# Kernel tuning notes

Hardware: AMD Instinct MI355X
Metric: run time of the kernel (lower is better)

The kernel has to match this reference:

```python
import jax, jax.numpy as jnp
import numpy as np

H = 2048          # hidden_size
F = 1408          # moe_intermediate_size
E = 64            # n_routed_experts
TOP_K = 6         # num_experts_per_tok
CAP = 512         # per-expert capacity (mean load ~192; overflow prob ~0)
SCALE = 1.0       # routed_scaling_factor
F_SH = 2 * F      # shared-expert intermediate (n_shared_experts=2)
B, S = 1, 2048


def setup_inputs() -> dict:
    key = jax.random.key(0)
    ks = jax.random.split(key, 8)
    s = 0.02
    return {
        "hidden_states": jax.random.normal(ks[0], (B, S, H), jnp.float32),
        "gate_w":  jax.random.normal(ks[1], (E, H), jnp.float32) * s,
        "w_gate":  jax.random.normal(ks[2], (E, H, F), jnp.float32) * s,
        "w_up":    jax.random.normal(ks[3], (E, H, F), jnp.float32) * s,
        "w_down":  jax.random.normal(ks[4], (E, F, H), jnp.float32) * s,
        "sh_gate": jax.random.normal(ks[5], (F_SH, H), jnp.float32) * s,
        "sh_up":   jax.random.normal(ks[6], (F_SH, H), jnp.float32) * s,
        "sh_down": jax.random.normal(ks[7], (H, F_SH), jnp.float32) * s,
    }


def reference(hidden_states, gate_w, w_gate, w_up, w_down, sh_gate, sh_up, sh_down):
    b, s, _ = hidden_states.shape
    x = hidden_states.reshape(-1, H)                       # [T, H]
    T = x.shape[0]

    # ---- gate: fp32 logits -> softmax -> top-k, scaled ----
    logits = x.astype(jnp.float32) @ gate_w.astype(jnp.float32).T   # [T, E]
    scores = jax.nn.softmax(logits, axis=-1)
    topk_w, topk_idx = jax.lax.top_k(scores, TOP_K)        # [T, K] (order irrelevant: summed)
    topk_w = topk_w * SCALE

    # ---- dispatch: sort expanded tokens by expert, scatter into [E, CAP, H] ----
    eid = topk_idx.reshape(-1)                             # [T*K]
    x_exp = jnp.repeat(x, TOP_K, axis=0)                   # [T*K, H] (token t repeated K times)
    order = jnp.argsort(eid)                               # stable sort by expert id
    eid_s = eid[order]
    counts = jnp.bincount(eid, length=E)
    starts = jnp.cumsum(counts) - counts                   # exclusive prefix sums
    pos = jnp.arange(T * TOP_K) - starts[eid_s]            # slot within expert
    valid = pos < CAP
    pos_c = jnp.where(valid, pos, CAP)                     # overflow -> scratch slot CAP
    buf = jnp.zeros((E, CAP + 1, H), x.dtype).at[eid_s, pos_c].set(x_exp[order])

    # ---- grouped expert SwiGLU MLP (grouped GEMM as batched einsum) ----
    g = jax.nn.silu(jnp.einsum('ech,ehf->ecf', buf, w_gate))
    u = jnp.einsum('ech,ehf->ecf', buf, w_up)
    d = jnp.einsum('ecf,efh->ech', g * u, w_down)          # [E, CAP+1, H]

    # ---- combine: gather, unsort, weighted sum over top-k ----
    out_s = jnp.where(valid[:, None], d[eid_s, pos_c], 0.0)
    out_exp = jnp.zeros_like(out_s).at[order].set(out_s)   # reverse_shuffle
    y = jnp.einsum('tkh,tk->th', out_exp.reshape(T, TOP_K, H), topk_w)
    y = y.astype(x.dtype).reshape(b, s, H)

    # ---- shared experts residual (dense SwiGLU MLP on identity) ----
    gs = jax.nn.silu(hidden_states @ sh_gate.T)
    us = hidden_states @ sh_up.T
    y = y + (gs * us) @ sh_down.T
    return y
```

## Files before the change

kernel.cpp:

```cpp
#include <hip/hip_runtime.h>
#include <hip/hip_bf16.h>

#define H 2048
#define FDIM 1408
#define NE 64
#define CAP 512
#define NTOK 2048
#define FSH 2816

typedef float  f32x4  __attribute__((ext_vector_type(4)));
typedef short  s16x8  __attribute__((ext_vector_type(8)));
typedef unsigned short u16;
typedef u16    u16x4v __attribute__((ext_vector_type(4)));

__device__ __forceinline__ u16 f2bf(float f) {
    union { float f; unsigned u; } v; v.f = f;
    unsigned u = v.u;
    u += 0x7fffu + ((u >> 16) & 1u);
    return (u16)(u >> 16);
}
__device__ __forceinline__ float bf2f(u16 b) {
    union { unsigned u; float f; } v; v.u = ((unsigned)b) << 16;
    return v.f;
}
__device__ __forceinline__ int swze(int row) {
    return (((row & 7) ^ ((row >> 3) & 7)) << 3);
}
__device__ __forceinline__ void wr4(u16* dst, float a, float b, float c, float d) {
    u16x4v v; v[0] = f2bf(a); v[1] = f2bf(b); v[2] = f2bf(c); v[3] = f2bf(d);
    *(u16x4v*)dst = v;
}

__global__ __launch_bounds__(256) void xcvt(const float* __restrict__ x, u16* __restrict__ xb) {
    int i = blockIdx.x * 256 + threadIdx.x;
    const float4 a = ((const float4*)x)[2 * i];
    const float4 b = ((const float4*)x)[2 * i + 1];
    u16 v[8] = { f2bf(a.x), f2bf(a.y), f2bf(a.z), f2bf(a.w),
                 f2bf(b.x), f2bf(b.y), f2bf(b.z), f2bf(b.w) };
    *(s16x8*)(xb + (size_t)i * 8) = *(s16x8*)v;
}

__global__ void init_cnt(int* __restrict__ c) { c[threadIdx.x] = 0; }

__global__ __launch_bounds__(64) void gate_topk(
    const float* __restrict__ xg, const float* __restrict__ gw,
    int* __restrict__ cnt, int* __restrict__ tok_of,
    int* __restrict__ slot_enc, float* __restrict__ tw)
{
    const int t = blockIdx.x;
    const int lane = threadIdx.x;
    __shared__ float4 xs[512];
    const float4* xr = (const float4*)(xg + (size_t)t * H);
    #pragma unroll
    for (int i = 0; i < 8; ++i) xs[i * 64 + lane] = xr[i * 64 + lane];
    __syncthreads();

    const float4* gr = (const float4*)(gw + (size_t)lane * H);
    float acc = 0.f;
    #pragma unroll 4
    for (int i = 0; i < 512; ++i) {
        float4 a = xs[i], b = gr[i];
        acc += a.x * b.x + a.y * b.y + a.z * b.z + a.w * b.w;
    }
    float m = acc;
    #pragma unroll
    for (int off = 32; off; off >>= 1) m = fmaxf(m, __shfl_xor(m, off));
    float p = __expf(acc - m);
    float s = p;
    #pragma unroll
    for (int off = 32; off; off >>= 1) s += __shfl_xor(s, off);
    p = p / s;

    float myw = 0.f; int mye = 0;
    float v = p;
    for (int k = 0; k < 6; ++k) {
        float bv = v; int bi = lane;
        #pragma unroll
        for (int off = 32; off; off >>= 1) {
            float ov = __shfl_xor(bv, off);
            int   oi = __shfl_xor(bi, off);
            if (ov > bv || (ov == bv && oi < bi)) { bv = ov; bi = oi; }
        }
        if (lane == k)  { myw = bv; mye = bi; }
        if (lane == bi) v = -1.f;
    }
    if (lane < 6) {
        int slot = atomicAdd(&cnt[mye], 1);
        int enc = -1;
        if (slot < CAP) { tok_of[mye * CAP + slot] = t; enc = mye * CAP + slot; }
        slot_enc[t * 6 + lane] = enc;
        tw[t * 6 + lane] = myw;
    }
}

template<bool ROUTED>
__global__ __launch_bounds__(256) void dual_gemm(
    const u16* __restrict__ xbf, const int* __restrict__ tok_of,
    const int* __restrict__ cnt_arr, const float* __restrict__ wg,
    const float* __restrict__ wu, u16* __restrict__ act, int Fd)
{
    __shared__ u16 As[256 * 64];
    __shared__ u16 Bgs[32 * 64];
    __shared__ u16 Bus[32 * 64];

    const int e = blockIdx.z;
    int cnt;
    if constexpr (ROUTED) { cnt = cnt_arr[e]; cnt = cnt < CAP ? cnt : CAP; }
    else cnt = NTOK;
    const int m0 = blockIdx.y * 256;
    if (m0 >= cnt) return;
    const int f0 = blockIdx.x * 32;

    const float* wg_e = wg;
    const float* wu_e = wu;
    u16* act_e = act;
    const int* tok = nullptr;
    if constexpr (ROUTED) {
        wg_e += (size_t)e * H * Fd;
        wu_e += (size_t)e * H * Fd;
        act_e += (size_t)e * CAP * Fd;
        tok = tok_of + e * CAP;
    }

    const int tid = threadIdx.x;
    const int lane = tid & 63;
    const int wv = tid >> 6;

    const int ac = tid & 7;
    const u16* arow[8];
    int arl[8];
    #pragma unroll
    for (int it = 0; it < 8; ++it) {
        int row = it * 32 + (tid >> 3);
        arl[it] = row;
        int srow = m0 + row;
        int tkn;
        if constexpr (ROUTED) tkn = (srow < cnt) ? tok[srow] : 0;
        else tkn = srow;
        arow[it] = xbf + (size_t)tkn * H;
    }
    const int bb = tid & 127;
    const int bn4 = bb & 7;
    const int bkb = bb >> 3;
    const float* bsrcR = ((tid < 128) ? wg_e : wu_e) + (size_t)f0 + bn4 * 4 + (size_t)bkb * 4 * Fd;
    const int dr = bb >> 2;
    const int dc = (bb & 3) * 4;
    const float* bsrcD = ((tid < 128) ? wg_e : wu_e) + (size_t)(f0 + dr) * H + dc * 4;

    f32x4 accg[4][2], accu[4][2];
    const f32x4 zero4 = {0.f, 0.f, 0.f, 0.f};
    #pragma unroll
    for (int i = 0; i < 4; ++i)
        #pragma unroll
        for (int j = 0; j < 2; ++j) { accg[i][j] = zero4; accu[i][j] = zero4; }

    s16x8 aR[8];
    float4 bR[4];

    #pragma unroll
    for (int it = 0; it < 8; ++it) aR[it] = *(const s16x8*)(arow[it] + ac * 8);
    if constexpr (ROUTED) {
        #pragma unroll
        for (int r = 0; r < 4; ++r) bR[r] = *(const float4*)(bsrcR + (size_t)r * Fd);
    } else {
        #pragma unroll
        for (int q = 0; q < 4; ++q) bR[q] = *(const float4*)(bsrcD + q * 4);
    }

    for (int kt = 0; kt < H / 64; ++kt) {
        #pragma unroll
        for (int it = 0; it < 8; ++it)
            *(s16x8*)&As[arl[it] * 64 + ((ac * 8) ^ swze(arl[it]))] = aR[it];
        u16* Bdst = (tid < 128) ? Bgs : Bus;
        if constexpr (ROUTED) {
            #pragma unroll
            for (int j = 0; j < 4; ++j) {
                int rr = bn4 * 4 + j;
                wr4(&Bdst[rr * 64 + ((bkb * 4) ^ swze(rr))], bR[0][j], bR[1][j], bR[2][j], bR[3][j]);
            }
        } else {
            #pragma unroll
            for (int q = 0; q < 4; ++q)
                wr4(&Bdst[dr * 64 + (((dc + q) * 4) ^ swze(dr))], bR[q].x, bR[q].y, bR[q].z, bR[q].w);
        }
        __syncthreads();

        if (kt + 1 < H / 64) {
            const int ko = (kt + 1) * 64;
            #pragma unroll
            for (int it = 0; it < 8; ++it) aR[it] = *(const s16x8*)(arow[it] + ko + ac * 8);
            if constexpr (ROUTED) {
                #pragma unroll
                for (int r = 0; r < 4; ++r) bR[r] = *(const float4*)(bsrcR + (size_t)(ko + r) * Fd);
            } else {
                #pragma unroll
                for (int q = 0; q < 4; ++q) bR[q] = *(const float4*)(bsrcD + ko + q * 4);
            }
        }

        __builtin_amdgcn_s_setprio(1);
        #pragma unroll
        for (int kk = 0; kk < 2; ++kk) {
            int ko = kk * 32 + (lane >> 4) * 8;
            s16x8 a[4], bg[2], bu[2];
            #pragma unroll
            for (int mi = 0; mi < 4; ++mi) {
                int r = wv * 64 + mi * 16 + (lane & 15);
                a[mi] = *(const s16x8*)&As[r * 64 + (ko ^ swze(r))];
            }
            #pragma unroll
            for (int ni = 0; ni < 2; ++ni) {
                int r = ni * 16 + (lane & 15);
                bg[ni] = *(const s16x8*)&Bgs[r * 64 + (ko ^ swze(r))];
                bu[ni] = *(const s16x8*)&Bus[r * 64 + (ko ^ swze(r))];
            }
            #pragma unroll
            for (int mi = 0; mi < 4; ++mi)
                #pragma unroll
                for (int ni = 0; ni < 2; ++ni) {
                    accg[mi][ni] = __builtin_amdgcn_mfma_f32_16x16x32_bf16(a[mi], bg[ni], accg[mi][ni], 0, 0, 0);
                    accu[mi][ni] = __builtin_amdgcn_mfma_f32_16x16x32_bf16(a[mi], bu[ni], accu[mi][ni], 0, 0, 0);
                }
        }
        __builtin_amdgcn_s_setprio(0);
        __syncthreads();
    }

    #pragma unroll
    for (int mi = 0; mi < 4; ++mi)
        #pragma unroll
        for (int ni = 0; ni < 2; ++ni)
            #pragma unroll
            for (int r = 0; r < 4; ++r) {
                int srow = m0 + wv * 64 + mi * 16 + (lane >> 4) * 4 + r;
                if (srow < cnt) {
                    int fc = f0 + ni * 16 + (lane & 15);
                    float g = accg[mi][ni][r], u = accu[mi][ni][r];
                    float aa = (g / (1.f + __expf(-g))) * u;
                    int fs = (fc & ~63) | ((fc & 63) ^ swze(srow));
                    act_e[(size_t)srow * Fd + fs] = f2bf(aa);
                }
            }
}

template<bool ROUTED>
__global__ __launch_bounds__(256) void down_gemm(
    const u16* __restrict__ actA, const float* __restrict__ wdn,
    void* __restrict__ outp, const int* __restrict__ cnt_arr, int Kd)
{
    __shared__ u16 As[256 * 64];
    __shared__ u16 Bs[64 * 64];

    const int e = blockIdx.z;
    int cnt;
    if constexpr (ROUTED) { cnt = cnt_arr[e]; cnt = cnt < CAP ? cnt : CAP; }
    else cnt = NTOK;
    const int m0 = blockIdx.y * 256;
    if (m0 >= cnt) return;
    const int n0 = blockIdx.x * 64;

    const u16* A_e = actA;
    const float* B_e = wdn;
    if constexpr (ROUTED) {
        A_e += (size_t)e * CAP * Kd;
        B_e += (size_t)e * Kd * H;
    }

    const int tid = threadIdx.x, lane = tid & 63, wv = tid >> 6;
    const int NT = Kd / 64;

    const int ac = tid & 7;
    int arl[8];
    const u16* arow[8];
    #pragma unroll
    for (int it = 0; it < 8; ++it) {
        int row = it * 32 + (tid >> 3);
        arl[it] = row;
        arow[it] = A_e + (size_t)(m0 + row) * Kd;
    }
    const int bn4 = tid & 15;
    const int bkb = tid >> 4;
    const float* bsrcR = B_e + (size_t)n0 + bn4 * 4 + (size_t)bkb * 4 * H;
    const int dr = tid >> 2;
    const int dc = (tid & 3) * 4;
    const float* bsrcD = B_e + (size_t)(n0 + dr) * FSH + dc * 4;

    f32x4 acc[4][4];
    const f32x4 zero4 = {0.f, 0.f, 0.f, 0.f};
    #pragma unroll
    for (int i = 0; i < 4; ++i)
        #pragma unroll
        for (int j = 0; j < 4; ++j) acc[i][j] = zero4;

    s16x8 aR[8];
    float4 bR[4];

    #pragma unroll
    for (int it = 0; it < 8; ++it) aR[it] = *(const s16x8*)(arow[it] + ac * 8);
    if constexpr (ROUTED) {
        #pragma unroll
        for (int r = 0; r < 4; ++r) bR[r] = *(const float4*)(bsrcR + (size_t)r * H);
    } else {
        #pragma unroll
        for (int q = 0; q < 4; ++q) bR[q] = *(const float4*)(bsrcD + q * 4);
    }

    for (int kt = 0; kt < NT; ++kt) {
        #pragma unroll
        for (int it = 0; it < 8; ++it)
            *(s16x8*)&As[arl[it] * 64 + (ac * 8)] = aR[it];
        if constexpr (ROUTED) {
            #pragma unroll
            for (int j = 0; j < 4; ++j) {
                int rr = bn4 * 4 + j;
                wr4(&Bs[rr * 64 + ((bkb * 4) ^ swze(rr))], bR[0][j], bR[1][j], bR[2][j], bR[3][j]);
            }
        } else {
            #pragma unroll
            for (int q = 0; q < 4; ++q)
                wr4(&Bs[dr * 64 + (((dc + q) * 4) ^ swze(dr))], bR[q].x, bR[q].y, bR[q].z, bR[q].w);
        }
        __syncthreads();

        if (kt + 1 < NT) {
            const int ko = (kt + 1) * 64;
            #pragma unroll
            for (int it = 0; it < 8; ++it) aR[it] = *(const s16x8*)(arow[it] + ko + ac * 8);
            if constexpr (ROUTED) {
                #pragma unroll
                for (int r = 0; r < 4; ++r) bR[r] = *(const float4*)(bsrcR + (size_t)(ko + r) * H);
            } else {
                #pragma unroll
                for (int q = 0; q < 4; ++q) bR[q] = *(const float4*)(bsrcD + ko + q * 4);
            }
        }

        __builtin_amdgcn_s_setprio(1);
        #pragma unroll
        for (int kk = 0; kk < 2; ++kk) {
            int ko = kk * 32 + (lane >> 4) * 8;
            s16x8 a[4], b[4];
            #pragma unroll
            for (int mi = 0; mi < 4; ++mi) {
                int r = wv * 64 + mi * 16 + (lane & 15);
                a[mi] = *(const s16x8*)&As[r * 64 + (ko ^ swze(r))];
            }
            #pragma unroll
            for (int ni = 0; ni < 4; ++ni) {
                int r = ni * 16 + (lane & 15);
                b[ni] = *(const s16x8*)&Bs[r * 64 + (ko ^ swze(r))];
            }
            #pragma unroll
            for (int mi = 0; mi < 4; ++mi)
                #pragma unroll
                for (int ni = 0; ni < 4; ++ni)
                    acc[mi][ni] = __builtin_amdgcn_mfma_f32_16x16x32_bf16(a[mi], b[ni], acc[mi][ni], 0, 0, 0);
        }
        __builtin_amdgcn_s_setprio(0);
        __syncthreads();
    }

    #pragma unroll
    for (int mi = 0; mi < 4; ++mi)
        #pragma unroll
        for (int ni = 0; ni < 4; ++ni)
            #pragma unroll
            for (int r = 0; r < 4; ++r) {
                int srow = m0 + wv * 64 + mi * 16 + (lane >> 4) * 4 + r;
                if (srow < cnt) {
                    int col = n0 + ni * 16 + (lane & 15);
                    float vv = acc[mi][ni][r];
                    if constexpr (ROUTED)
                        ((u16*)outp)[(size_t)e * CAP * H + (size_t)srow * H + col] = f2bf(vv);
                    else
                        ((float*)outp)[(size_t)srow * H + col] = vv;
                }
            }
}

__global__ __launch_bounds__(256) void combine(
    float* __restrict__ y, const u16* __restrict__ d,
    const int* __restrict__ slot_enc, const float* __restrict__ tw)
{
    const int t = blockIdx.x, tid = threadIdx.x;
    int enc[6]; float w[6];
    #pragma unroll
    for (int k = 0; k < 6; ++k) {
        enc[k] = slot_enc[t * 6 + k];
        w[k] = tw[t * 6 + k];
    }
    float4* yrow = (float4*)(y + (size_t)t * H);
    #pragma unroll
    for (int it = 0; it < 2; ++it) {
        int h4 = it * 256 + tid;
        float4 acc = yrow[h4];
        #pragma unroll
        for (int k = 0; k < 6; ++k) {
            if (enc[k] >= 0) {
                ushort4 dv = ((const ushort4*)(d + (size_t)enc[k] * H))[h4];
                acc.x += w[k] * bf2f(dv.x);
                acc.y += w[k] * bf2f(dv.y);
                acc.z += w[k] * bf2f(dv.z);
                acc.w += w[k] * bf2f(dv.w);
            }
        }
        yrow[h4] = acc;
    }
}

extern "C" void kernel_launch(void* const* d_in, const int* in_sizes, int n_in,
                              void* d_out, int out_size, void* d_ws, size_t ws_size,
                              hipStream_t stream) {
    const float* x       = (const float*)d_in[0];
    const float* gw      = (const float*)d_in[1];
    const float* w_gate  = (const float*)d_in[2];
    const float* w_up    = (const float*)d_in[3];
    const float* w_down  = (const float*)d_in[4];
    const float* sh_gate = (const float*)d_in[5];
    const float* sh_up   = (const float*)d_in[6];
    const float* sh_down = (const float*)d_in[7];
    float* y = (float*)d_out;

    char* wsb = (char*)d_ws;
    int*   cnt      = (int*)(wsb + 0);
    int*   tok_of   = (int*)(wsb + 512);
    int*   slot_enc = (int*)(wsb + 512 + 131072);
    float* tw       = (float*)(wsb + 512 + 131072 + 49152);
    u16*   act      = (u16*)(wsb + 230144);
    u16*   actsh    = (u16*)(wsb + 230144 + 92274688);
    u16*   dbuf     = (u16*)(wsb + 230144 + 92274688 + 11534336);
    u16*   xbf      = dbuf;

    init_cnt<<<1, 64, 0, stream>>>(cnt);
    xcvt<<<NTOK * H / 8 / 256, 256, 0, stream>>>(x, xbf);
    gate_topk<<<NTOK, 64, 0, stream>>>(x, gw, cnt, tok_of, slot_enc, tw);
    dual_gemm<true><<<dim3(FDIM / 32, 2, NE), 256, 0, stream>>>(
        xbf, tok_of, cnt, w_gate, w_up, act, FDIM);
    dual_gemm<false><<<dim3(FSH / 32, NTOK / 256, 1), 256, 0, stream>>>(
        xbf, nullptr, nullptr, sh_gate, sh_up, actsh, FSH);
    down_gemm<true><<<dim3(H / 64, 2, NE), 256, 0, stream>>>(
        act, w_down, (void*)dbuf, cnt, FDIM);
    down_gemm<false><<<dim3(H / 64, NTOK / 256, 1), 256, 0, stream>>>(
        actsh, sh_down, (void*)y, nullptr, FSH);
    combine<<<NTOK, 256, 0, stream>>>(y, dbuf, slot_enc, tw);
}
```

Before: 937.0 us.

## Double-buffer LDS tiles with k-major layout and two-deep register prefetch in GEMMs

Both the dual (gate/up) and down GEMM kernels now keep two LDS buffers. The loop stores the next tile while computing the current one and loads tile kt+2 into registers, which removes one barrier per k-step. The LDS layout moves from row-major with an XOR swizzle to a k8-major [k8][row][8] layout with XOR on the B rows. Each thread now loads one full A row, which drops the swizzled activation output, and the shared-expert grids are transposed so M blocks vary fastest for weight reuse. The cost is doubled LDS use, which may reduce occupancy despite the launch_bounds hint of 2 blocks, plus a custom barrier that waits only on lgkmcnt.

New measurement: 1.107 ms. 1.18x slower.

```diff
diff --git a/kernel.cpp b/kernel.cpp
--- a/kernel.cpp
+++ b/kernel.cpp
@@ -23,13 +23,9 @@
     union { unsigned u; float f; } v; v.u = ((unsigned)b) << 16;
     return v.f;
 }
-__device__ __forceinline__ int swze(int row) {
-    return (((row & 7) ^ ((row >> 3) & 7)) << 3);
-}
-__device__ __forceinline__ void wr4(u16* dst, float a, float b, float c, float d) {
-    u16x4v v; v[0] = f2bf(a); v[1] = f2bf(b); v[2] = f2bf(c); v[3] = f2bf(d);
-    *(u16x4v*)dst = v;
-}
+
+#define BAR() do { asm volatile("s_waitcnt lgkmcnt(0)" ::: "memory"); \
+                   __builtin_amdgcn_s_barrier(); } while (0)
 
 __global__ __launch_bounds__(256) void xcvt(const float* __restrict__ x, u16* __restrict__ xb) {
     int i = blockIdx.x * 256 + threadIdx.x;
@@ -94,59 +90,62 @@
 }
 
 template<bool ROUTED>
-__global__ __launch_bounds__(256) void dual_gemm(
+__global__ __launch_bounds__(256, 2) void dual_gemm(
     const u16* __restrict__ xbf, const int* __restrict__ tok_of,
     const int* __restrict__ cnt_arr, const float* __restrict__ wg,
     const float* __restrict__ wu, u16* __restrict__ act, int Fd)
 {
-    __shared__ u16 As[256 * 64];
-    __shared__ u16 Bgs[32 * 64];
-    __shared__ u16 Bus[32 * 64];
-
-    const int e = blockIdx.z;
-    int cnt;
-    if constexpr (ROUTED) { cnt = cnt_arr[e]; cnt = cnt < CAP ? cnt : CAP; }
-    else cnt = NTOK;
-    const int m0 = blockIdx.y * 256;
-    if (m0 >= cnt) return;
-    const int f0 = blockIdx.x * 32;
+    __shared__ u16 As[2][8][256][8];
+    __shared__ u16 Bs[2][2][8][32][8];
+
+    int e = 0, cnt, m0, f0;
+    if constexpr (ROUTED) {
+        e = blockIdx.z;
+        cnt = cnt_arr[e]; cnt = cnt < CAP ? cnt : CAP;
+        f0 = blockIdx.x * 32; m0 = blockIdx.y * 256;
+        if (m0 >= cnt) return;
+    } else {
+        cnt = NTOK;
+        m0 = blockIdx.x * 256; f0 = blockIdx.y * 32;
+    }
 
     const float* wg_e = wg;
     const float* wu_e = wu;
     u16* act_e = act;
-    const int* tok = nullptr;
     if constexpr (ROUTED) {
         wg_e += (size_t)e * H * Fd;
         wu_e += (size_t)e * H * Fd;
         act_e += (size_t)e * CAP * Fd;
-        tok = tok_of + e * CAP;
     }
 
     const int tid = threadIdx.x;
     const int lane = tid & 63;
     const int wv = tid >> 6;
 
-    const int ac = tid & 7;
-    const u16* arow[8];
-    int arl[8];
-    #pragma unroll
-    for (int it = 0; it < 8; ++it) {
-        int row = it * 32 + (tid >> 3);
-        arl[it] = row;
-        int srow = m0 + row;
-        int tkn;
-        if constexpr (ROUTED) tkn = (srow < cnt) ? tok[srow] : 0;
-        else tkn = srow;
-        arow[it] = xbf + (size_t)tkn * H;
-    }
+    const u16* aptr;
+    {
+        int srow = m0 + tid;
+        if constexpr (ROUTED) {
+            const int* tok = tok_of + e * CAP;
+            aptr = xbf + (size_t)tok[srow < cnt ? srow : 0] * H;
+        } else {
+            aptr = xbf + (size_t)srow * H;
+        }
+    }
+    const int mat = tid >> 7;
     const int bb = tid & 127;
-    const int bn4 = bb & 7;
-    const int bkb = bb >> 3;
-    const float* bsrcR = ((tid < 128) ? wg_e : wu_e) + (size_t)f0 + bn4 * 4 + (size_t)bkb * 4 * Fd;
-    const int dr = bb >> 2;
-    const int dc = (bb & 3) * 4;
-    const float* bsrcD = ((tid < 128) ? wg_e : wu_e) + (size_t)(f0 + dr) * H + dc * 4;
-
+    const float* bsrc;
+    int n4 = 0, kq = 0, br = 0, bc = 0;
+    if constexpr (ROUTED) {
+        n4 = bb & 7; kq = bb >> 3;
+        bsrc = (mat ? wu_e : wg_e) + (size_t)(kq * 4) * Fd + f0 + n4 * 4;
+    } else {
+        br = bb >> 2; bc = bb & 3;
+        bsrc = (mat ? wu_e : wg_e) + (size_t)(f0 + br) * H + bc * 16;
+    }
+
+    s16x8 aR[8];
+    f32x4 bR[4];
     f32x4 accg[4][2], accu[4][2];
     const f32x4 zero4 = {0.f, 0.f, 0.f, 0.f};
     #pragma unroll
@@ -154,65 +153,62 @@
         #pragma unroll
         for (int j = 0; j < 2; ++j) { accg[i][j] = zero4; accu[i][j] = zero4; }
 
-    s16x8 aR[8];
-    float4 bR[4];
-
-    #pragma unroll
-    for (int it = 0; it < 8; ++it) aR[it] = *(const s16x8*)(arow[it] + ac * 8);
-    if constexpr (ROUTED) {
-        #pragma unroll
-        for (int r = 0; r < 4; ++r) bR[r] = *(const float4*)(bsrcR + (size_t)r * Fd);
-    } else {
-        #pragma unroll
-        for (int q = 0; q < 4; ++q) bR[q] = *(const float4*)(bsrcD + q * 4);
-    }
-
+    auto LOAD = [&](int kt) {
+        #pragma unroll
+        for (int q = 0; q < 8; ++q) aR[q] = *(const s16x8*)(aptr + kt * 64 + q * 8);
+        if constexpr (ROUTED) {
+            #pragma unroll
+            for (int j = 0; j < 4; ++j)
+                bR[j] = *(const f32x4*)(bsrc + ((size_t)kt * 64 + j) * Fd);
+        } else {
+            #pragma unroll
+            for (int q = 0; q < 4; ++q)
+                bR[q] = *(const f32x4*)(bsrc + kt * 64 + q * 4);
+        }
+    };
+    auto STORE = [&](int b) {
+        #pragma unroll
+        for (int q = 0; q < 8; ++q) *(s16x8*)&As[b][q][tid][0] = aR[q];
+        if constexpr (ROUTED) {
+            const int k8 = kq >> 1, ko = (kq & 1) * 4;
+            #pragma unroll
+            for (int c = 0; c < 4; ++c) {
+                u16x4v v; v[0] = f2bf(bR[0][c]); v[1] = f2bf(bR[1][c]);
+                          v[2] = f2bf(bR[2][c]); v[3] = f2bf(bR[3][c]);
+                *(u16x4v*)&Bs[b][mat][k8][(n4 * 4 + c) ^ k8][ko] = v;
+            }
+        } else {
+            #pragma unroll
+            for (int h = 0; h < 2; ++h) {
+                const int k8 = bc * 2 + h;
+                u16 v[8];
+                f32x4 x0 = bR[h * 2], x1 = bR[h * 2 + 1];
+                v[0]=f2bf(x0[0]); v[1]=f2bf(x0[1]); v[2]=f2bf(x0[2]); v[3]=f2bf(x0[3]);
+                v[4]=f2bf(x1[0]); v[5]=f2bf(x1[1]); v[6]=f2bf(x1[2]); v[7]=f2bf(x1[3]);
+                *(s16x8*)&Bs[b][mat][k8][br ^ k8][0] = *(s16x8*)v;
+            }
+        }
+    };
+
+    LOAD(0); STORE(0); LOAD(1);
+    BAR();
     for (int kt = 0; kt < H / 64; ++kt) {
-        #pragma unroll
-        for (int it = 0; it < 8; ++it)
-            *(s16x8*)&As[arl[it] * 64 + ((ac * 8) ^ swze(arl[it]))] = aR[it];
-        u16* Bdst = (tid < 128) ? Bgs : Bus;
-        if constexpr (ROUTED) {
-            #pragma unroll
-            for (int j = 0; j < 4; ++j) {
-                int rr = bn4 * 4 + j;
-                wr4(&Bdst[rr * 64 + ((bkb * 4) ^ swze(rr))], bR[0][j], bR[1][j], bR[2][j], bR[3][j]);
-            }
-        } else {
-            #pragma unroll
-            for (int q = 0; q < 4; ++q)
-                wr4(&Bdst[dr * 64 + (((dc + q) * 4) ^ swze(dr))], bR[q].x, bR[q].y, bR[q].z, bR[q].w);
-        }
-        __syncthreads();
-
-        if (kt + 1 < H / 64) {
-            const int ko = (kt + 1) * 64;
-            #pragma unroll
-            for (int it = 0; it < 8; ++it) aR[it] = *(const s16x8*)(arow[it] + ko + ac * 8);
-            if constexpr (ROUTED) {
-                #pragma unroll
-                for (int r = 0; r < 4; ++r) bR[r] = *(const float4*)(bsrcR + (size_t)(ko + r) * Fd);
-            } else {
-                #pragma unroll
-                for (int q = 0; q < 4; ++q) bR[q] = *(const float4*)(bsrcD + ko + q * 4);
-            }
-        }
-
+        const int b = kt & 1;
+        if (kt + 1 < H / 64) STORE(b ^ 1);
+        if (kt + 2 < H / 64) LOAD(kt + 2);
         __builtin_amdgcn_s_setprio(1);
         #pragma unroll
         for (int kk = 0; kk < 2; ++kk) {
-            int ko = kk * 32 + (lane >> 4) * 8;
+            const int k8 = kk * 4 + (lane >> 4);
             s16x8 a[4], bg[2], bu[2];
             #pragma unroll
-            for (int mi = 0; mi < 4; ++mi) {
-                int r = wv * 64 + mi * 16 + (lane & 15);
-                a[mi] = *(const s16x8*)&As[r * 64 + (ko ^ swze(r))];
-            }
+            for (int mi = 0; mi < 4; ++mi)
+                a[mi] = *(const s16x8*)&As[b][k8][wv * 64 + mi * 16 + (lane & 15)][0];
             #pragma unroll
             for (int ni = 0; ni < 2; ++ni) {
-                int r = ni * 16 + (lane & 15);
-                bg[ni] = *(const s16x8*)&Bgs[r * 64 + (ko ^ swze(r))];
-                bu[ni] = *(const s16x8*)&Bus[r * 64 + (ko ^ swze(r))];
+                const int np = (ni * 16 + (lane & 15)) ^ k8;
+                bg[ni] = *(const s16x8*)&Bs[b][0][k8][np][0];
+                bu[ni] = *(const s16x8*)&Bs[b][1][k8][np][0];
             }
             #pragma unroll
             for (int mi = 0; mi < 4; ++mi)
@@ -223,7 +219,7 @@
                 }
         }
         __builtin_amdgcn_s_setprio(0);
-        __syncthreads();
+        BAR();
     }
 
     #pragma unroll
@@ -237,27 +233,29 @@
                     int fc = f0 + ni * 16 + (lane & 15);
                     float g = accg[mi][ni][r], u = accu[mi][ni][r];
                     float aa = (g / (1.f + __expf(-g))) * u;
-                    int fs = (fc & ~63) | ((fc & 63) ^ swze(srow));
-                    act_e[(size_t)srow * Fd + fs] = f2bf(aa);
+                    act_e[(size_t)srow * Fd + fc] = f2bf(aa);
                 }
             }
 }
 
 template<bool ROUTED>
-__global__ __launch_bounds__(256) void down_gemm(
+__global__ __launch_bounds__(256, 2) void down_gemm(
     const u16* __restrict__ actA, const float* __restrict__ wdn,
     void* __restrict__ outp, const int* __restrict__ cnt_arr, int Kd)
 {
-    __shared__ u16 As[256 * 64];
-    __shared__ u16 Bs[64 * 64];
-
-    const int e = blockIdx.z;
-    int cnt;
-    if constexpr (ROUTED) { cnt = cnt_arr[e]; cnt = cnt < CAP ? cnt : CAP; }
-    else cnt = NTOK;
-    const int m0 = blockIdx.y * 256;
-    if (m0 >= cnt) return;
-    const int n0 = blockIdx.x * 64;
+    __shared__ u16 As[2][8][256][8];
+    __shared__ u16 Bs[2][8][64][8];
+
+    int e = 0, cnt, m0, n0;
+    if constexpr (ROUTED) {
+        e = blockIdx.z;
+        cnt = cnt_arr[e]; cnt = cnt < CAP ? cnt : CAP;
+        n0 = blockIdx.x * 64; m0 = blockIdx.y * 256;
+        if (m0 >= cnt) return;
+    } else {
+        cnt = NTOK;
+        m0 = blockIdx.x * 256; n0 = blockIdx.y * 64;
+    }
 
     const u16* A_e = actA;
     const float* B_e = wdn;
@@ -265,26 +263,27 @@
         A_e += (size_t)e * CAP * Kd;
         B_e += (size_t)e * Kd * H;
     }
-
+    const int NT = Kd / 64;
     const int tid = threadIdx.x, lane = tid & 63, wv = tid >> 6;
-    const int NT = Kd / 64;
-
-    const int ac = tid & 7;
-    int arl[8];
-    const u16* arow[8];
-    #pragma unroll
-    for (int it = 0; it < 8; ++it) {
-        int row = it * 32 + (tid >> 3);
-        arl[it] = row;
-        arow[it] = A_e + (size_t)(m0 + row) * Kd;
-    }
-    const int bn4 = tid & 15;
-    const int bkb = tid >> 4;
-    const float* bsrcR = B_e + (size_t)n0 + bn4 * 4 + (size_t)bkb * 4 * H;
-    const int dr = tid >> 2;
-    const int dc = (tid & 3) * 4;
-    const float* bsrcD = B_e + (size_t)(n0 + dr) * FSH + dc * 4;
-
+
+    const u16* aptr;
+    {
+        int row = m0 + tid;
+        if constexpr (ROUTED) aptr = A_e + (size_t)(row < cnt ? row : m0) * Kd;
+        else aptr = A_e + (size_t)row * Kd;
+    }
+    const float* bsrc;
+    int n4 = 0, kq = 0, br = 0, bc = 0;
+    if constexpr (ROUTED) {
+        n4 = tid & 15; kq = tid >> 4;
+        bsrc = B_e + (size_t)(kq * 4) * H + n0 + n4 * 4;
+    } else {
+        br = tid >> 2; bc = tid & 3;
+        bsrc = B_e + (size_t)(n0 + br) * FSH + bc * 16;
+    }
+
+    s16x8 aR[8];
+    f32x4 bR[4];
     f32x4 acc[4][4];
     const f32x4 zero4 = {0.f, 0.f, 0.f, 0.f};
     #pragma unroll
@@ -292,72 +291,68 @@
         #pragma unroll
         for (int j = 0; j < 4; ++j) acc[i][j] = zero4;
 
-    s16x8 aR[8];
-    float4 bR[4];
-
-    #pragma unroll
-    for (int it = 0; it < 8; ++it) aR[it] = *(const s16x8*)(arow[it] + ac * 8);
-    if constexpr (ROUTED) {
-        #pragma unroll
-        for (int r = 0; r < 4; ++r) bR[r] = *(const float4*)(bsrcR + (size_t)r * H);
-    } else {
-        #pragma unroll
-        for (int q = 0; q < 4; ++q) bR[q] = *(const float4*)(bsrcD + q * 4);
-    }
-
+    auto LOAD = [&](int kt) {
+        #pragma unroll
+        for (int q = 0; q < 8; ++q) aR[q] = *(const s16x8*)(aptr + kt * 64 + q * 8);
+        if constexpr (ROUTED) {
+            #pragma unroll
+            for (int j = 0; j < 4; ++j)
+                bR[j] = *(const f32x4*)(bsrc + ((size_t)kt * 64 + j) * H);
+        } else {
+            #pragma unroll
+            for (int q = 0; q < 4; ++q)
+                bR[q] = *(const f32x4*)(bsrc + kt * 64 + q * 4);
+        }
+    };
+    auto STORE = [&](int b) {
+        #pragma unroll
+        for (int q = 0; q < 8; ++q) *(s16x8*)&As[b][q][tid][0] = aR[q];
+        if constexpr (ROUTED) {
+            const int k8 = kq >> 1, ko = (kq & 1) * 4;
+            #pragma unroll
+            for (int c = 0; c < 4; ++c) {
+                u16x4v v; v[0] = f2bf(bR[0][c]); v[1] = f2bf(bR[1][c]);
+                          v[2] = f2bf(bR[2][c]); v[3] = f2bf(bR[3][c]);
+                *(u16x4v*)&Bs[b][k8][(n4 * 4 + c) ^ k8][ko] = v;
+            }
+        } else {
+            #pragma unroll
+            for (int h = 0; h < 2; ++h) {
+                const int k8 = bc * 2 + h;
+                u16 v[8];
+                f32x4 x0 = bR[h * 2], x1 = bR[h * 2 + 1];
+                v[0]=f2bf(x0[0]); v[1]=f2bf(x0[1]); v[2]=f2bf(x0[2]); v[3]=f2bf(x0[3]);
+                v[4]=f2bf(x1[0]); v[5]=f2bf(x1[1]); v[6]=f2bf(x1[2]); v[7]=f2bf(x1[3]);
+                *(s16x8*)&Bs[b][k8][br ^ k8][0] = *(s16x8*)v;
+            }
+        }
+    };
+
+    LOAD(0); STORE(0); LOAD(1);
+    BAR();
     for (int kt = 0; kt < NT; ++kt) {
-        #pragma unroll
-        for (int it = 0; it < 8; ++it)
-            *(s16x8*)&As[arl[it] * 64 + (ac * 8)] = aR[it];
-        if constexpr (ROUTED) {
-            #pragma unroll
-            for (int j = 0; j < 4; ++j) {
-                int rr = bn4 * 4 + j;
-                wr4(&Bs[rr * 64 + ((bkb * 4) ^ swze(rr))], bR[0][j], bR[1][j], bR[2][j], bR[3][j]);
-            }
-        } else {
-            #pragma unroll
-            for (int q = 0; q < 4; ++q)
-                wr4(&Bs[dr * 64 + (((dc + q) * 4) ^ swze(dr))], bR[q].x, bR[q].y, bR[q].z, bR[q].w);
-        }
-        __syncthreads();
-
-        if (kt + 1 < NT) {
-            const int ko = (kt + 1) * 64;
-            #pragma unroll
-            for (int it = 0; it < 8; ++it) aR[it] = *(const s16x8*)(arow[it] + ko + ac * 8);
-            if constexpr (ROUTED) {
-                #pragma unroll
-                for (int r = 0; r < 4; ++r) bR[r] = *(const float4*)(bsrcR + (size_t)(ko + r) * H);
-            } else {
-                #pragma unroll
-                for (int q = 0; q < 4; ++q) bR[q] = *(const float4*)(bsrcD + ko + q * 4);
-            }
-        }
-
+        const int b = kt & 1;
+        if (kt + 1 < NT) STORE(b ^ 1);
+        if (kt + 2 < NT) LOAD(kt + 2);
         __builtin_amdgcn_s_setprio(1);
         #pragma unroll
         for (int kk = 0; kk < 2; ++kk) {
-            int ko = kk * 32 + (lane >> 4) * 8;
-            s16x8 a[4], b[4];
-            #pragma unroll
-            for (int mi = 0; mi < 4; ++mi) {
-                int r = wv * 64 + mi * 16 + (lane & 15);
-                a[mi] = *(const s16x8*)&As[r * 64 + (ko ^ swze(r))];
-            }
-            #pragma unroll
-            for (int ni = 0; ni < 4; ++ni) {
-                int r = ni * 16 + (lane & 15);
-                b[ni] = *(const s16x8*)&Bs[r * 64 + (ko ^ swze(r))];
-            }
+            const int k8 = kk * 4 + (lane >> 4);
+            s16x8 a[4], bf[4];
+            #pragma unroll
+            for (int mi = 0; mi < 4; ++mi)
+                a[mi] = *(const s16x8*)&As[b][k8][wv * 64 + mi * 16 + (lane & 15)][0];
+            #pragma unroll
+            for (int ni = 0; ni < 4; ++ni)
+                bf[ni] = *(const s16x8*)&Bs[b][k8][(ni * 16 + (lane & 15)) ^ k8][0];
             #pragma unroll
             for (int mi = 0; mi < 4; ++mi)
                 #pragma unroll
                 for (int ni = 0; ni < 4; ++ni)
-                    acc[mi][ni] = __builtin_amdgcn_mfma_f32_16x16x32_bf16(a[mi], b[ni], acc[mi][ni], 0, 0, 0);
+                    acc[mi][ni] = __builtin_amdgcn_mfma_f32_16x16x32_bf16(a[mi], bf[ni], acc[mi][ni], 0, 0, 0);
         }
         __builtin_amdgcn_s_setprio(0);
-        __syncthreads();
+        BAR();
     }
 
     #pragma unroll
@@ -436,11 +431,11 @@
     gate_topk<<<NTOK, 64, 0, stream>>>(x, gw, cnt, tok_of, slot_enc, tw);
     dual_gemm<true><<<dim3(FDIM / 32, 2, NE), 256, 0, stream>>>(
         xbf, tok_of, cnt, w_gate, w_up, act, FDIM);
-    dual_gemm<false><<<dim3(FSH / 32, NTOK / 256, 1), 256, 0, stream>>>(
+    dual_gemm<false><<<dim3(NTOK / 256, FSH / 32, 1), 256, 0, stream>>>(
         xbf, nullptr, nullptr, sh_gate, sh_up, actsh, FSH);
     down_gemm<true><<<dim3(H / 64, 2, NE), 256, 0, stream>>>(
         act, w_down, (void*)dbuf, cnt, FDIM);
-    down_gemm<false><<<dim3(H / 64, NTOK / 256, 1), 256, 0, stream>>>(
+    down_gemm<false><<<dim3(NTOK / 256, H / 64, 1), 256, 0, stream>>>(
         actsh, sh_down, (void*)y, nullptr, FSH);
     combine<<<NTOK, 256, 0, stream>>>(y, dbuf, slot_enc, tw);
 }
```
